# Performance work log

Hardware: AMD Instinct MI355X
Metric: run time of the kernel (lower is better)

The kernel has to match this reference:

```python
import math
import jax, jax.numpy as jnp
import numpy as np


def _precompute_psi(nlat_in, nlon_in, nlat_out, K, theta_cutoff):
    """Faithful numpy port of _precompute_convolution_tensor (equiangular grids).
    Returns COO indices (k, t, lat_in, lon_in) and float values of the sparse
    filter tensor psi of logical shape [K, nlat_out, nlat_in*nlon_in]."""
    lats_in = np.linspace(0.0, np.pi, nlat_in)
    lats_out = np.linspace(0.0, np.pi, nlat_out)
    phis = np.linspace(-np.pi, np.pi, nlon_in)
    d_theta = theta_cutoff / K
    theta_i = np.arange(K) * d_theta  # (K,)
    ks, ts, las, los, vs = [], [], [], [], []
    alpha = -lats_in[:, None]          # (nlat_in, 1)
    beta = phis[None, :]               # (1, nlon_in)
    for t in range(nlat_out):
        gamma = lats_out[t]
        z = np.cos(alpha) * np.cos(gamma) - np.cos(beta) * np.sin(alpha) * np.sin(gamma)
        theta = np.arccos(np.clip(z, -1.0, 1.0))   # (nlat_in, nlon_in)
        diff = np.abs(theta[None, :, :] - theta_i[:, None, None])  # (K, nlat_in, nlon_in)
        mask = (diff < d_theta) & (theta[None, :, :] < theta_cutoff)
        k_idx, la_idx, lo_idx = np.nonzero(mask)
        v = 1.0 - diff[k_idx, la_idx, lo_idx] / d_theta  # triangle (hat) weights
        ks.append(k_idx); ts.append(np.full_like(k_idx, t)); las.append(la_idx); los.append(lo_idx); vs.append(v)
    return (np.concatenate(ks).astype(np.int32),
            np.concatenate(ts).astype(np.int32),
            np.concatenate(las).astype(np.int32),
            np.concatenate(los).astype(np.int32),
            np.concatenate(vs).astype(np.float32))


def setup_inputs() -> dict:
    B, C = 4, 32
    nlat_in, nlon_in = 361, 720
    nlat_out, nlon_out = 361, 720
    K = 3
    theta_cutoff = 0.01 * math.pi  # default used at the precompute call site
    k, t, la, lo, v = _precompute_psi(nlat_in, nlon_in, nlat_out, K, theta_cutoff)
    key = jax.random.key(0)
    x = jax.random.normal(key, (B, C, nlat_in, nlon_in), dtype=jnp.float32)
    return {
        "x": x,
        "psi_vals": jnp.asarray(v),
        "psi_k": jnp.asarray(k),
        "psi_t": jnp.asarray(t),
        "psi_lat": jnp.asarray(la),
        "psi_lon": jnp.asarray(lo),
        "kernel_size": K,
        "nlat_out": nlat_out,
        "nlon_out": nlon_out,
    }


def reference(x, psi_vals, psi_k, psi_t, psi_lat, psi_lon, kernel_size, nlat_out, nlon_out):
    B, C, nlat_in, nlon_in = x.shape
    BC = B * C
    scale = nlon_in // nlon_out  # = 1 here
    # (nlat_in, nlon_in, BC) layout, matching x.reshape(B*C,...).permute(1,2,0)
    xr = x.reshape(BC, nlat_in, nlon_in).transpose(1, 2, 0)
    seg = psi_k * nlat_out + psi_t           # row id in the (K*nlat_out) output
    num_seg = kernel_size * nlat_out

    def step(_, p):
        # torch.roll(x, scale, dims=lon) applied (p+1) times before the bmm:
        # rolled[lat, lon] = x[lat, (lon - (p+1)*scale) % nlon]
        lon_idx = (psi_lon - (p + 1) * scale) % nlon_in
        g = xr[psi_lat, lon_idx]             # (nnz, BC) irregular gather
        out_p = jax.ops.segment_sum(psi_vals[:, None] * g, seg, num_segments=num_seg)
        return None, out_p                   # (K*nlat_out, BC)

    _, outs = jax.lax.scan(step, None, jnp.arange(nlon_out))  # (nlon_out, K*nlat_out, BC)
    outs = outs.reshape(nlon_out, kernel_size, nlat_out, BC)
    # permute(3,1,2,0) then split BC -> (B, C)
    return outs.transpose(3, 1, 2, 0).reshape(B, C, kernel_size, nlat_out, nlon_out)
```

## Files before the change

### kernel.cpp

```cpp
#include <hip/hip_runtime.h>
#include <math.h>


#define NLAT 361
#define NLON 720
#define KK 3
#define PTILE 48
#define NT 384
#define SWN 832
#define TOTCAP (720*1024)

typedef __attribute__((ext_vector_type(8))) short bf16x8;
typedef __attribute__((ext_vector_type(4))) float f32x4;
typedef __attribute__((ext_vector_type(4))) unsigned int u32x4;

#define D_PI 3.14159265358979311599796346854418516159057617187500
#define STEP_LAT (D_PI / 360.0)
#define STEP_PHI ((2.0 * D_PI) / 719.0)
#define CUTOFF (0.01 * D_PI)
#define DTH (CUTOFF / 3.0)

__device__ inline unsigned int bf16pair_rne(float lo, float hi) {
    unsigned int a = __builtin_bit_cast(unsigned int, lo);
    unsigned int b = __builtin_bit_cast(unsigned int, hi);
    a = a + 0x7fffu + ((a >> 16) & 1u);
    b = b + 0x7fffu + ((b >> 16) & 1u);
    return (a >> 16) | (b & 0xffff0000u);
}

__global__ __launch_bounds__(512) void bounds_kernel(int4* __restrict__ params,
                                                     float2* __restrict__ pAB,
                                                     unsigned long long* __restrict__ actd) {
    __shared__ int part[512];
    int tid = threadIdx.x;
    int rmins[9], Ws[9], bl8s[9];
    float As[9], Bs[9];
    int wsum = 0;
    if (tid < NLAT) {
        int t = tid;
        double g = (t == 360) ? D_PI : (double)t * STEP_LAT;
        double cg = cos(g), sg = sin(g);
        const double coscut = cos(CUTOFF);
#pragma unroll
        for (int d = 0; d < 9; ++d) {
            int la = t + d - 4;
            int rmin = 0, W = 0;
            double A = 0.0, Bc = 0.0;
            if (la >= 0 && la <= 360) {
                double lad = (la == 360) ? D_PI : (double)la * STEP_LAT;
                A = cos(lad) * cg;
                Bc = sin(lad) * sg;
                if (Bc < 1e-14) {
                    if (A > coscut) { rmin = 0; W = 720; }
                } else {
                    double C = (coscut - A) / Bc;
                    if (C <= -1.0) { rmin = 0; W = 720; }
                    else if (C < 1.0) {
                        double bmax = acos(C);
                        int r0 = (int)floor((D_PI - bmax) / STEP_PHI) + 1;
                        int r1 = (int)ceil((D_PI + bmax) / STEP_PHI) - 1;
                        if (r0 < 0) r0 = 0;
                        if (r1 > 719) r1 = 719;
                        rmin = r0; W = r1 - r0 + 1;
                        if (W < 0) W = 0;
                    }
                }
            }
            rmins[d] = rmin; Ws[d] = W;
            As[d] = (float)A; Bs[d] = (float)Bc;
            int b8 = (W > 0) ? ((W + 104 + 7) & ~7) : 0;
            bl8s[d] = b8;
            wsum += b8;
        }
    }
    part[tid] = wsum;
    __syncthreads();
    for (int dd = 1; dd < 512; dd <<= 1) {
        int v = part[tid];
        int w2 = (tid >= dd) ? part[tid - dd] : 0;
        __syncthreads();
        part[tid] = v + w2;
        __syncthreads();
    }
    int base = part[tid] - wsum;
    if (tid < NLAT) {
        unsigned long long pk = 0;
        int nact = 0;
#pragma unroll
        for (int d = 0; d < 9; ++d) {
            int off = base;
            base += bl8s[d];
            if (Ws[d] > 0 && off + bl8s[d] <= TOTCAP) {
                params[tid * 9 + d] = make_int4(rmins[d], Ws[d], off, bl8s[d]);
                pAB[tid * 9 + d] = make_float2(As[d], Bs[d]);
                pk |= ((unsigned long long)d) << (4 + 4 * nact);
                nact++;
            } else {
                params[tid * 9 + d] = make_int4(0, 0, 0, 0);
            }
        }
        pk |= (unsigned long long)nact;
        actd[tid] = pk;
    }
}

__global__ __launch_bounds__(128) void fill_w_kernel(const int4* __restrict__ params,
                                                     const float2* __restrict__ pAB,
                                                     unsigned int* __restrict__ wtab) {
    int row = blockIdx.x;
    int4 pr = params[row];
    int W = pr.y;
    if (W <= 0) return;
    int rmin = pr.x, off = pr.z, bl8 = pr.w;
    float2 ab = pAB[row];
    float A = ab.x, Bc = ab.y;
    const float invd = (float)(1.0 / DTH);
    for (int idx = threadIdx.x; idx < bl8; idx += 128) {
        int j = idx - 56;
        float f1 = 1.0e9f, f2 = 1.0e9f;
        if (j >= 0 && j < W) {
            int lo = rmin + j;
            float beta = (lo == 719) ? (float)D_PI : (float)((double)lo * STEP_PHI - D_PI);
            float z = fminf(1.f, fmaxf(-1.f, fmaf(Bc, cosf(beta), A)));
            f1 = acosf(z) * invd;
        }
        if (j + 1 >= 0 && j + 1 < W) {
            int lo = rmin + j + 1;
            float beta = (lo == 719) ? (float)D_PI : (float)((double)lo * STEP_PHI - D_PI);
            float z = fminf(1.f, fmaxf(-1.f, fmaf(Bc, cosf(beta), A)));
            f2 = acosf(z) * invd;
        }
        float w0a = fmaxf(0.f, 1.f - f1);
        float w1a = fmaxf(0.f, 1.f - fabsf(f1 - 1.f));
        float w2a = fmaxf(0.f, 1.f - fabsf(f1 - 2.f));
        float w0b = fmaxf(0.f, 1.f - f2);
        float w1b = fmaxf(0.f, 1.f - fabsf(f2 - 1.f));
        float w2b = fmaxf(0.f, 1.f - fabsf(f2 - 2.f));
        wtab[0 * TOTCAP + off + idx] = bf16pair_rne(w0a, w0b);
        wtab[1 * TOTCAP + off + idx] = bf16pair_rne(w1a, w1b);
        wtab[2 * TOTCAP + off + idx] = bf16pair_rne(w2a, w2b);
    }
}

__global__ void cvt_x_kernel(const float* __restrict__ x, unsigned int* __restrict__ xb,
                             int n8) {
    for (int i = blockIdx.x * 256 + threadIdx.x; i < n8; i += gridDim.x * 256) {
        f32x4 a = *(const f32x4*)(x + (size_t)i * 8);
        f32x4 b = *(const f32x4*)(x + (size_t)i * 8 + 4);
        u32x4 q;
        q.x = bf16pair_rne(a.x, a.y);
        q.y = bf16pair_rne(a.z, a.w);
        q.z = bf16pair_rne(b.x, b.y);
        q.w = bf16pair_rne(b.z, b.w);
        *(u32x4*)(xb + (size_t)i * 4) = q;
    }
}

template <int USEBF16>
__global__ __launch_bounds__(NT, 3) void dconv_mfma_kernel(
    const float* __restrict__ x, const unsigned short* __restrict__ xb,
    const int4* __restrict__ params, const unsigned long long* __restrict__ actd,
    const unsigned int* __restrict__ wtab, float* __restrict__ out) {
    __shared__ __attribute__((aligned(16))) unsigned char sB[128 * 128];
    __shared__ unsigned int sWi[KK * SWN];

    int orig = blockIdx.x;
    int y = orig / 15, px = orig % 15;
    int t = (y & 1) ? (360 - (y >> 1)) : (y >> 1);
    int p0 = px * PTILE;
    int tid = threadIdx.x;
    int lane = tid & 63;
    int w = tid >> 6;
    int psub = w >> 1;
    int bc0w = (w & 1) * 64;
    int l15 = lane & 15;
    int l4 = lane >> 4;

    f32x4 acc[4][KK];
#pragma unroll
    for (int n = 0; n < 4; ++n)
#pragma unroll
        for (int k = 0; k < KK; ++k) acc[n][k] = (f32x4){0.f, 0.f, 0.f, 0.f};

    unsigned long long pk = actd[t];
    int nact = (int)(pk & 15ull);

    int c = 0, iact = 0;
    int la = 0, rmin = 0, W = 0, off = 0, bl8 = 0, mbase = 0, shift = 0;
    int nK = 0, nC = 1, ks_lo = 0, ks_hi = -1;

    unsigned int wra[3], wrb[3], wrc[3];
    u32x4 br[3];

    auto LOADP = [&](int dd) {
        la = t + dd - 4;
        int4 pr = params[t * 9 + dd];
        rmin = pr.x; W = pr.y; off = pr.z; bl8 = pr.w;
        int ms0 = rmin - 48 - p0;
        shift = (ms0 + 720) & 7;
        nK = (W + 47 + shift + 31) >> 5;
        nC = (nK + 1) >> 1;
        mbase = (((ms0 - shift) % 720) + 720) % 720;
        int s_off = psub * 16 + 9 - shift;
        int kl = (9 - s_off + 31) >> 5;
        ks_lo = kl < 0 ? 0 : kl;
        int kh = (55 + W - s_off) >> 5;
        ks_hi = kh > nK - 1 ? nK - 1 : kh;
    };
    auto ISSUE_W = [&]() {
#pragma unroll
        for (int pass = 0; pass < 3; ++pass) {
            int idx = pass * NT + tid;
            bool g2 = idx < bl8;
            wra[pass] = g2 ? wtab[0 * TOTCAP + off + idx] : 0u;
            wrb[pass] = g2 ? wtab[1 * TOTCAP + off + idx] : 0u;
            wrc[pass] = g2 ? wtab[2 * TOTCAP + off + idx] : 0u;
        }
    };
    auto WRITE_W = [&]() {
#pragma unroll
        for (int pass = 0; pass < 3; ++pass) {
            int idx = pass * NT + tid;
            if (idx < bl8) {
                sWi[0 * SWN + idx] = wra[pass];
                sWi[1 * SWN + idx] = wrb[pass];
                sWi[2 * SWN + idx] = wrc[pass];
            }
        }
    };
    auto ISSUE_B = [&](int cc) {
#pragma unroll
        for (int pass = 0; pass < 3; ++pass) {
            int slot = pass * NT + tid;
            if (slot < 1024) {
                int bc = slot >> 3;
                int mo = (slot & 7) * 8;
                int mg = mbase + cc * 64 + mo;
                mg -= (mg >= 720) ? 720 : 0;
                mg -= (mg >= 720) ? 720 : 0;
                mg -= (mg >= 720) ? 720 : 0;
                if (USEBF16) {
                    br[pass] = *(const u32x4*)(xb + ((size_t)bc * NLAT + la) * NLON + mg);
                } else {
                    const float* src = x + ((size_t)bc * NLAT + la) * NLON + mg;
                    f32x4 a = *(const f32x4*)(src);
                    f32x4 b = *(const f32x4*)(src + 4);
                    u32x4 q;
                    q.x = bf16pair_rne(a.x, a.y);
                    q.y = bf16pair_rne(a.z, a.w);
                    q.z = bf16pair_rne(b.x, b.y);
                    q.w = bf16pair_rne(b.z, b.w);
                    br[pass] = q;
                }
            }
        }
    };
    auto WRITE_B = [&]() {
#pragma unroll
        for (int pass = 0; pass < 3; ++pass) {
            int slot = pass * NT + tid;
            if (slot < 1024) {
                int bc = slot >> 3;
                int mo = (slot & 7) * 8;
                int cw = (mo * 2) ^ ((bc & 7) << 4);
                *(u32x4*)(sB + bc * 128 + cw) = br[pass];
            }
        }
    };

    LOADP((int)((pk >> 4) & 15ull));
    ISSUE_W();
    ISSUE_B(0);

    while (true) {
        __syncthreads();
        if (c == 0) WRITE_W();
        WRITE_B();
        __syncthreads();
        int shiftS = shift;
        int c2 = c * 2;
        int kloS = ks_lo > c2 ? ks_lo : c2;
        int khiS = ks_hi < c2 + 1 ? ks_hi : c2 + 1;
        bool done = false;
        if (c + 1 < nC) {
            c = c + 1;
            ISSUE_B(c);
        } else if (iact + 1 < nact) {
            iact++;
            c = 0;
            LOADP((int)((pk >> (4 + 4 * iact)) & 15ull));
            ISSUE_W();
            ISSUE_B(0);
        } else {
            done = true;
        }
        int soffS = psub * 16 + 9 - shiftS;
        for (int ks = kloS; ks <= khiS; ++ks) {
            int ksl = ks - c2;
            int s = ks * 32 + l4 * 8 + soffS + l15;
            bf16x8 af[KK];
#pragma unroll
            for (int k = 0; k < KK; ++k) {
                const unsigned int* wp = sWi + k * SWN + s;
                u32x4 q;
                q.x = wp[0];
                q.y = wp[2];
                q.z = wp[4];
                q.w = wp[6];
                af[k] = __builtin_bit_cast(bf16x8, q);
            }
            int colbase = ksl * 64 + l4 * 16;
#pragma unroll
            for (int n = 0; n < 4; ++n) {
                int brow = bc0w + n * 16 + l15;
                int colb = colbase ^ ((brow & 7) << 4);
                bf16x8 bfv = *(const bf16x8*)(sB + brow * 128 + colb);
                acc[n][0] = __builtin_amdgcn_mfma_f32_16x16x32_bf16(af[0], bfv, acc[n][0], 0, 0, 0);
                acc[n][1] = __builtin_amdgcn_mfma_f32_16x16x32_bf16(af[1], bfv, acc[n][1], 0, 0, 0);
                acc[n][2] = __builtin_amdgcn_mfma_f32_16x16x32_bf16(af[2], bfv, acc[n][2], 0, 0, 0);
            }
        }
        if (done) break;
    }

    int p = p0 + psub * 16 + l4 * 4;
#pragma unroll
    for (int n = 0; n < 4; ++n) {
        int bc = bc0w + n * 16 + l15;
#pragma unroll
        for (int k = 0; k < KK; ++k) {
            float* o = out + (((size_t)bc * KK + k) * NLAT + t) * NLON + p;
            *(f32x4*)o = acc[n][k];
        }
    }
}

extern "C" void kernel_launch(void* const* d_in, const int* in_sizes, int n_in,
                              void* d_out, int out_size, void* d_ws, size_t ws_size,
                              hipStream_t stream) {
    const float* x = (const float*)d_in[0];
    float* out = (float*)d_out;

    char* ws = (char*)d_ws;
    int4* params = (int4*)(ws + 0);
    float2* pAB = (float2*)(ws + 53248);
    unsigned long long* actd = (unsigned long long*)(ws + 81920);
    unsigned int* wtab = (unsigned int*)(ws + 90112);
    size_t xb_off = (90112 + (size_t)3 * TOTCAP * 4 + 4095) & ~(size_t)4095;
    size_t xb_bytes = (size_t)128 * NLAT * NLON * 2;
    int use_bf16 = (ws_size >= xb_off + xb_bytes) ? 1 : 0;
    unsigned short* xb = (unsigned short*)(ws + xb_off);

    bounds_kernel<<<1, 512, 0, stream>>>(params, pAB, actd);
    fill_w_kernel<<<NLAT * 9, 128, 0, stream>>>(params, pAB, wtab);

    dim3 grid(15 * NLAT, 1, 1);
    if (use_bf16) {
        int n8 = 128 * NLAT * NLON / 8;
        cvt_x_kernel<<<2048, 256, 0, stream>>>(x, (unsigned int*)xb, n8);
        dconv_mfma_kernel<1><<<grid, NT, 0, stream>>>(x, xb, params, actd, wtab, out);
    } else {
        dconv_mfma_kernel<0><<<grid, NT, 0, stream>>>(x, xb, params, actd, wtab, out);
    }
}
```

Before: 319.4 us.

## Widen lon tile to 80 with 5 waves each covering all 128 channels

Raises the longitude tile from 48 to 80 outputs per block. Each of the 5 waves now covers the full 128 BC channels with 8 accumulator groups, instead of splitting channels across wave pairs. The grid is remapped to 9 lon tiles, with blocks for 8 latitude rows interleaved, and the weight padding and strip bounds are adjusted to match. This amortizes the x strip and weight loads over more outputs, cutting redundant halo traffic. The cost is more registers and occupancy dropping to 2 blocks per CU. Nontemporal loads in the convert kernel and nontemporal output stores are also added to reduce cache pollution.

```diff
diff --git a/kernel.cpp b/kernel.cpp
--- a/kernel.cpp
+++ b/kernel.cpp
@@ -5,9 +5,11 @@
 #define NLAT 361
 #define NLON 720
 #define KK 3
-#define PTILE 48
-#define NT 384
-#define SWN 832
+#define PTILE 80
+#define NPX 9
+#define NT 320
+#define PD 88
+#define SWN 896
 #define TOTCAP (720*1024)
 
 typedef __attribute__((ext_vector_type(8))) short bf16x8;
@@ -68,7 +70,11 @@
             }
             rmins[d] = rmin; Ws[d] = W;
             As[d] = (float)A; Bs[d] = (float)Bc;
-            int b8 = (W > 0) ? ((W + 104 + 7) & ~7) : 0;
+            int b8 = 0;
+            if (W > 0) {
+                b8 = (W + 175) & ~7;
+                if (b8 > SWN) b8 = SWN;
+            }
             bl8s[d] = b8;
             wsum += b8;
         }
@@ -116,7 +122,7 @@
     float A = ab.x, Bc = ab.y;
     const float invd = (float)(1.0 / DTH);
     for (int idx = threadIdx.x; idx < bl8; idx += 128) {
-        int j = idx - 56;
+        int j = idx - PD;
         float f1 = 1.0e9f, f2 = 1.0e9f;
         if (j >= 0 && j < W) {
             int lo = rmin + j;
@@ -145,8 +151,8 @@
 __global__ void cvt_x_kernel(const float* __restrict__ x, unsigned int* __restrict__ xb,
                              int n8) {
     for (int i = blockIdx.x * 256 + threadIdx.x; i < n8; i += gridDim.x * 256) {
-        f32x4 a = *(const f32x4*)(x + (size_t)i * 8);
-        f32x4 b = *(const f32x4*)(x + (size_t)i * 8 + 4);
+        f32x4 a = __builtin_nontemporal_load((const f32x4*)(x + (size_t)i * 8));
+        f32x4 b = __builtin_nontemporal_load((const f32x4*)(x + (size_t)i * 8 + 4));
         u32x4 q;
         q.x = bf16pair_rne(a.x, a.y);
         q.y = bf16pair_rne(a.z, a.w);
@@ -157,28 +163,31 @@
 }
 
 template <int USEBF16>
-__global__ __launch_bounds__(NT, 3) void dconv_mfma_kernel(
+__global__ __launch_bounds__(NT, 2) void dconv_mfma_kernel(
     const float* __restrict__ x, const unsigned short* __restrict__ xb,
     const int4* __restrict__ params, const unsigned long long* __restrict__ actd,
     const unsigned int* __restrict__ wtab, float* __restrict__ out) {
     __shared__ __attribute__((aligned(16))) unsigned char sB[128 * 128];
     __shared__ unsigned int sWi[KK * SWN];
 
-    int orig = blockIdx.x;
-    int y = orig / 15, px = orig % 15;
-    int t = (y & 1) ? (360 - (y >> 1)) : (y >> 1);
+    int bid = blockIdx.x;
+    int r = bid & 7;
+    int rest = bid >> 3;
+    int px = rest % 9;
+    int q = rest / 9;
+    int yp = 8 * q + r;
+    if (yp > 360) return;
+    int t = (yp & 1) ? (360 - (yp >> 1)) : (yp >> 1);
     int p0 = px * PTILE;
     int tid = threadIdx.x;
     int lane = tid & 63;
-    int w = tid >> 6;
-    int psub = w >> 1;
-    int bc0w = (w & 1) * 64;
+    int psub = tid >> 6;
     int l15 = lane & 15;
     int l4 = lane >> 4;
 
-    f32x4 acc[4][KK];
-#pragma unroll
-    for (int n = 0; n < 4; ++n)
+    f32x4 acc[8][KK];
+#pragma unroll
+    for (int n = 0; n < 8; ++n)
 #pragma unroll
         for (int k = 0; k < KK; ++k) acc[n][k] = (f32x4){0.f, 0.f, 0.f, 0.f};
 
@@ -186,25 +195,26 @@
     int nact = (int)(pk & 15ull);
 
     int c = 0, iact = 0;
-    int la = 0, rmin = 0, W = 0, off = 0, bl8 = 0, mbase = 0, shift = 0;
+    int la = 0, W = 0, off = 0, bl8 = 0, mbase = 0, shift = 0;
     int nK = 0, nC = 1, ks_lo = 0, ks_hi = -1;
 
     unsigned int wra[3], wrb[3], wrc[3];
-    u32x4 br[3];
+    u32x4 br[4];
 
     auto LOADP = [&](int dd) {
         la = t + dd - 4;
         int4 pr = params[t * 9 + dd];
-        rmin = pr.x; W = pr.y; off = pr.z; bl8 = pr.w;
-        int ms0 = rmin - 48 - p0;
+        int rmin = pr.x;
+        W = pr.y; off = pr.z; bl8 = pr.w;
+        int ms0 = rmin - PTILE - p0;
         shift = (ms0 + 720) & 7;
-        nK = (W + 47 + shift + 31) >> 5;
+        nK = (W + 79 + shift + 31) >> 5;
         nC = (nK + 1) >> 1;
         mbase = (((ms0 - shift) % 720) + 720) % 720;
         int s_off = psub * 16 + 9 - shift;
-        int kl = (9 - s_off + 31) >> 5;
+        int kl = (73 - s_off) >> 5;
         ks_lo = kl < 0 ? 0 : kl;
-        int kh = (55 + W - s_off) >> 5;
+        int kh = (87 + W - s_off) >> 5;
         ks_hi = kh > nK - 1 ? nK - 1 : kh;
     };
     auto ISSUE_W = [&]() {
@@ -230,7 +240,7 @@
     };
     auto ISSUE_B = [&](int cc) {
 #pragma unroll
-        for (int pass = 0; pass < 3; ++pass) {
+        for (int pass = 0; pass < 4; ++pass) {
             int slot = pass * NT + tid;
             if (slot < 1024) {
                 int bc = slot >> 3;
@@ -245,19 +255,19 @@
                     const float* src = x + ((size_t)bc * NLAT + la) * NLON + mg;
                     f32x4 a = *(const f32x4*)(src);
                     f32x4 b = *(const f32x4*)(src + 4);
-                    u32x4 q;
-                    q.x = bf16pair_rne(a.x, a.y);
-                    q.y = bf16pair_rne(a.z, a.w);
-                    q.z = bf16pair_rne(b.x, b.y);
-                    q.w = bf16pair_rne(b.z, b.w);
-                    br[pass] = q;
+                    u32x4 qq;
+                    qq.x = bf16pair_rne(a.x, a.y);
+                    qq.y = bf16pair_rne(a.z, a.w);
+                    qq.z = bf16pair_rne(b.x, b.y);
+                    qq.w = bf16pair_rne(b.z, b.w);
+                    br[pass] = qq;
                 }
             }
         }
     };
     auto WRITE_B = [&]() {
 #pragma unroll
-        for (int pass = 0; pass < 3; ++pass) {
+        for (int pass = 0; pass < 4; ++pass) {
             int slot = pass * NT + tid;
             if (slot < 1024) {
                 int bc = slot >> 3;
@@ -302,17 +312,17 @@
 #pragma unroll
             for (int k = 0; k < KK; ++k) {
                 const unsigned int* wp = sWi + k * SWN + s;
-                u32x4 q;
-                q.x = wp[0];
-                q.y = wp[2];
-                q.z = wp[4];
-                q.w = wp[6];
-                af[k] = __builtin_bit_cast(bf16x8, q);
+                u32x4 qf;
+                qf.x = wp[0];
+                qf.y = wp[2];
+                qf.z = wp[4];
+                qf.w = wp[6];
+                af[k] = __builtin_bit_cast(bf16x8, qf);
             }
             int colbase = ksl * 64 + l4 * 16;
 #pragma unroll
-            for (int n = 0; n < 4; ++n) {
-                int brow = bc0w + n * 16 + l15;
+            for (int n = 0; n < 8; ++n) {
+                int brow = n * 16 + l15;
                 int colb = colbase ^ ((brow & 7) << 4);
                 bf16x8 bfv = *(const bf16x8*)(sB + brow * 128 + colb);
                 acc[n][0] = __builtin_amdgcn_mfma_f32_16x16x32_bf16(af[0], bfv, acc[n][0], 0, 0, 0);
@@ -325,12 +335,12 @@
 
     int p = p0 + psub * 16 + l4 * 4;
 #pragma unroll
-    for (int n = 0; n < 4; ++n) {
-        int bc = bc0w + n * 16 + l15;
+    for (int n = 0; n < 8; ++n) {
+        int bc = n * 16 + l15;
 #pragma unroll
         for (int k = 0; k < KK; ++k) {
             float* o = out + (((size_t)bc * KK + k) * NLAT + t) * NLON + p;
-            *(f32x4*)o = acc[n][k];
+            __builtin_nontemporal_store(acc[n][k], (f32x4*)o);
         }
     }
 }
@@ -354,7 +364,7 @@
     bounds_kernel<<<1, 512, 0, stream>>>(params, pAB, actd);
     fill_w_kernel<<<NLAT * 9, 128, 0, stream>>>(params, pAB, wtab);
 
-    dim3 grid(15 * NLAT, 1, 1);
+    dim3 grid(8 * NPX * 46, 1, 1);
     if (use_bf16) {
         int n8 = 128 * NLAT * NLON / 8;
         cvt_x_kernel<<<2048, 256, 0, stream>>>(x, (unsigned int*)xb, n8);
```

Measured after the change: 345.8 us. 8.3% more time.
